# Performance work log

Hardware: AMD Instinct MI355X
Metric: run time of the kernel (lower is better)

Reference implementation:

```python
import jax, jax.numpy as jnp
import numpy as np

N = 100000       # nodes
E = 1600000      # edges
NFEAT = 256
NHID = 128
NCLASS = 40


def setup_inputs() -> dict:
    key = jax.random.key(0)
    ks = jax.random.split(key, 7)
    x = jax.random.normal(ks[0], (N, NFEAT), dtype=jnp.float32)
    edge_index = jax.random.randint(ks[1], (2, E), 0, N, dtype=jnp.int32)
    edge_weight = jax.random.uniform(ks[2], (E,), dtype=jnp.float32)
    # Glorot-style init as in PyG GCNConv.reset_parameters
    W1 = jax.random.normal(ks[3], (NFEAT, NHID), dtype=jnp.float32) * np.float32(1.0 / np.sqrt(NFEAT))
    b1 = jnp.zeros((NHID,), dtype=jnp.float32)
    W2 = jax.random.normal(ks[4], (NHID, NCLASS), dtype=jnp.float32) * np.float32(1.0 / np.sqrt(NHID))
    b2 = jnp.zeros((NCLASS,), dtype=jnp.float32)
    return {"x": x, "edge_index": edge_index, "edge_weight": edge_weight,
            "W1": W1, "b1": b1, "W2": W2, "b2": b2}


def gcn_conv(x, W, b, src, dst, ew, n):
    """PyG GCNConv with add_self_loops=True (self-loop weight 1), sym norm.

    Self-loop contribution is added analytically (norm_ii = deg_i^-1) so we
    never materialize the augmented edge list.
    """
    xw = x @ W                                            # [n, out]
    deg = jax.ops.segment_sum(ew, dst, num_segments=n) + 1.0  # +1 self loop
    dinv = jnp.where(deg > 0, jax.lax.rsqrt(deg), 0.0)    # deg^-1/2
    norm = dinv[src] * ew * dinv[dst]                     # [E]
    agg = jax.ops.segment_sum(norm[:, None] * xw[src], dst, num_segments=n)
    agg = agg + (dinv * dinv)[:, None] * xw               # self-loop term
    return agg + b


def reference(x, edge_index, edge_weight, W1, b1, W2, b2):
    n = x.shape[0]
    src, dst = edge_index[0], edge_index[1]
    h = jax.nn.relu(gcn_conv(x, W1, b1, src, dst, edge_weight, n))
    # dropout is identity in eval mode
    h = gcn_conv(h, W2, b2, src, dst, edge_weight, n)
    nrm = jnp.linalg.norm(h, axis=-1, keepdims=True)      # F.normalize p=2
    return h / jnp.maximum(nrm, 1e-12)
```

## Files before the change

kernel.cpp:

```cpp
#include <hip/hip_runtime.h>


typedef unsigned short u16;
typedef unsigned long long u64;
typedef __attribute__((ext_vector_type(8))) short short8;
typedef __attribute__((ext_vector_type(4))) float f32x4;

#define FIXSCALE 4194304.0f
#define HW2S 64
#define NSLAB 384
#define MAXBUCK 832

static __device__ inline u16 f2bf(float f) {
    unsigned u = __float_as_uint(f);
    return (u16)((u + 0x7fffu + ((u >> 16) & 1u)) >> 16);
}
static __device__ inline float bf2f(u16 h) { return __uint_as_float(((unsigned)h) << 16); }

__launch_bounds__(256)
__global__ void k_count(const int* __restrict__ dst, int* __restrict__ cnt1,
                        int E, int EPB, int NBUCK) {
    __shared__ int cnt[MAXBUCK];
    int b = blockIdx.x;
    for (int j = threadIdx.x; j < NBUCK; j += 256) cnt[j] = 0;
    __syncthreads();
    int beg = b * EPB, end = min(beg + EPB, E);
    for (int i = beg + threadIdx.x; i < end; i += 256)
        atomicAdd(&cnt[dst[i] >> 7], 1);
    __syncthreads();
    for (int j = threadIdx.x; j < NBUCK; j += 256)
        cnt1[(size_t)b * NBUCK + j] = cnt[j];
}

__launch_bounds__(NSLAB)
__global__ void k_s2a(int* __restrict__ cnt1, int* __restrict__ colTot, int NBUCK) {
    __shared__ int s[NSLAB];
    int j = blockIdx.x;
    int t = threadIdx.x;
    int v = cnt1[(size_t)t * NBUCK + j];
    s[t] = v;
    __syncthreads();
    for (int off = 1; off < NSLAB; off <<= 1) {
        int u = (t >= off) ? s[t - off] : 0;
        __syncthreads();
        s[t] += u;
        __syncthreads();
    }
    cnt1[(size_t)t * NBUCK + j] = s[t] - v;
    if (t == NSLAB - 1) colTot[j] = s[t];
}

__launch_bounds__(1024)
__global__ void k_s2b(const int* __restrict__ colTot, int* __restrict__ bucketBase,
                      int* __restrict__ rowp, int NBUCK, int N, int E) {
    __shared__ int s[1024];
    int t = threadIdx.x;
    int v = (t < NBUCK) ? colTot[t] : 0;
    s[t] = v;
    __syncthreads();
    for (int off = 1; off < 1024; off <<= 1) {
        int u = (t >= off) ? s[t - off] : 0;
        __syncthreads();
        s[t] += u;
        __syncthreads();
    }
    if (t < NBUCK) bucketBase[t] = s[t] - v;
    if (t == NBUCK - 1) bucketBase[NBUCK] = s[t];
    if (t == 0) rowp[N] = E;
}

__launch_bounds__(256)
__global__ void k_fat(const float* __restrict__ x, const u16* __restrict__ wt_hi,
                      u16* __restrict__ xw1, int N,
                      const int* __restrict__ src, const int* __restrict__ dst,
                      const float* __restrict__ ew, const int* __restrict__ cnt1,
                      const int* __restrict__ bucketBase, u64* __restrict__ tmp,
                      int E, int gB, int EPB, int NBUCK) {
    __shared__ __align__(16) u16 S[10240];
    u16* Ah = S;
    u16* Bh = S + 5120;

    if (blockIdx.x >= gB) {
        int* ldsOff = (int*)S;
        int b = blockIdx.x - gB, t = threadIdx.x;
        for (int j = t; j < NBUCK; j += 256)
            ldsOff[j] = bucketBase[j] + cnt1[(size_t)b * NBUCK + j];
        __syncthreads();
        int beg = b * EPB, end = min(beg + EPB, E);
        for (int i = beg + t; i < end; i += 256) {
            int d = dst[i];
            int slot = atomicAdd(&ldsOff[d >> 7], 1);
            unsigned fix = (unsigned)__float2uint_rn(ew[i] * FIXSCALE);
            tmp[slot] = ((u64)(unsigned)src[i] << 30) | ((u64)(d & 127) << 23) | fix;
        }
        return;
    }

    const int t = threadIdx.x;
    const int w = t >> 6;
    const int lane = t & 63;
    const int lrow = lane & 15;
    const int q = lane >> 4;
    const int lk = q * 8;
    const int row0 = blockIdx.x * 128;

    int rA[4], cA[4];
    const float* pA[4];
    bool okA[4];
#pragma unroll
    for (int i = 0; i < 4; ++i) {
        int flat = t + i * 256;
        rA[i] = flat >> 3;
        cA[i] = flat & 7;
        int gr = row0 + rA[i];
        okA[i] = gr < N;
        pA[i] = x + (size_t)min(gr, N - 1) * 256 + cA[i] * 4;
    }
    int nB[2], cB[2];
    const u16* pB[2];
#pragma unroll
    for (int i = 0; i < 2; ++i) {
        int flat = t + i * 256;
        nB[i] = flat >> 2;
        cB[i] = flat & 3;
        pB[i] = wt_hi + (size_t)nB[i] * 256 + cB[i] * 8;
    }

    float4 ra[4];
    short8 rb[2];
#pragma unroll
    for (int i = 0; i < 4; ++i)
        ra[i] = okA[i] ? *(const float4*)(pA[i]) : make_float4(0.f, 0.f, 0.f, 0.f);
#pragma unroll
    for (int i = 0; i < 2; ++i) rb[i] = *(const short8*)(pB[i]);

    f32x4 acc[2][8] = {};

    for (int kt = 0; kt < 8; ++kt) {
#pragma unroll
        for (int i = 0; i < 4; ++i) {
            ushort4 vh;
            vh.x = f2bf(ra[i].x);
            vh.y = f2bf(ra[i].y);
            vh.z = f2bf(ra[i].z);
            vh.w = f2bf(ra[i].w);
            *(ushort4*)(Ah + rA[i] * 40 + cA[i] * 4) = vh;
        }
#pragma unroll
        for (int i = 0; i < 2; ++i)
            *(short8*)(Bh + nB[i] * 40 + cB[i] * 8) = rb[i];
        __syncthreads();

        if (kt < 7) {
#pragma unroll
            for (int i = 0; i < 4; ++i)
                ra[i] = okA[i] ? *(const float4*)(pA[i] + (kt + 1) * 32)
                               : make_float4(0.f, 0.f, 0.f, 0.f);
#pragma unroll
            for (int i = 0; i < 2; ++i)
                rb[i] = *(const short8*)(pB[i] + (kt + 1) * 32);
        }

        short8 a0 = *(const short8*)(Ah + (w * 32 + lrow) * 40 + lk);
        short8 a1 = *(const short8*)(Ah + (w * 32 + 16 + lrow) * 40 + lk);
#pragma unroll
        for (int ni = 0; ni < 8; ++ni) {
            short8 bh = *(const short8*)(Bh + (ni * 16 + lrow) * 40 + lk);
            acc[0][ni] = __builtin_amdgcn_mfma_f32_16x16x32_bf16(a0, bh, acc[0][ni], 0, 0, 0);
            acc[1][ni] = __builtin_amdgcn_mfma_f32_16x16x32_bf16(a1, bh, acc[1][ni], 0, 0, 0);
        }
        __syncthreads();
    }

#pragma unroll
    for (int mi = 0; mi < 2; ++mi) {
        if (mi) __syncthreads();
#pragma unroll
        for (int r = 0; r < 4; ++r)
#pragma unroll
            for (int ni = 0; ni < 8; ++ni)
                S[(w * 16 + q * 4 + r) * 136 + lrow + ni * 16] = f2bf(acc[mi][ni][r]);
        __syncthreads();
        int l = t >> 2;
        int grow = row0 + (l >> 4) * 32 + mi * 16 + (l & 15);
        if (grow < N) {
#pragma unroll
            for (int c = 0; c < 4; ++c) {
                int col = (t & 3) * 8 + c * 32;
                *(short8*)(xw1 + (size_t)grow * 128 + col) =
                    *(const short8*)(S + l * 136 + col);
            }
        }
    }
}

__launch_bounds__(256)
__global__ void k_s4(const u64* __restrict__ tmp, const int* __restrict__ bucketBase,
                     int* __restrict__ rowp, float* __restrict__ dinv,
                     int2* __restrict__ entries, int N) {
    __shared__ int cnt[128];
    __shared__ unsigned degfix[128];
    __shared__ int sc[128];
    __shared__ int nextOff[128];
    __shared__ float dl[128];
    int k = blockIdx.x, t = threadIdx.x;
    int base = bucketBase[k], endb = bucketBase[k + 1];
    if (t < 128) { cnt[t] = 0; degfix[t] = 0; }
    __syncthreads();
    for (int i = base + t; i < endb; i += 256) {
        u64 r = tmp[i];
        int lid = (int)(r >> 23) & 127;
        atomicAdd(&cnt[lid], 1);
        atomicAdd(&degfix[lid], (unsigned)(r & 0x7fffff));
    }
    __syncthreads();
    if (t < 128) sc[t] = cnt[t];
    __syncthreads();
    for (int off = 1; off < 128; off <<= 1) {
        int u = 0;
        if (t < 128 && t >= off) u = sc[t - off];
        __syncthreads();
        if (t < 128) sc[t] += u;
        __syncthreads();
    }
    if (t < 128) {
        int off0 = base + sc[t] - cnt[t];
        nextOff[t] = off0;
        float di = rsqrtf((float)degfix[t] * (1.0f / FIXSCALE) + 1.0f);
        dl[t] = di;
        int gn = k * 128 + t;
        if (gn < N) { rowp[gn] = off0; dinv[gn] = di; }
    }
    __syncthreads();
    for (int i = base + t; i < endb; i += 256) {
        u64 r = tmp[i];
        int lid = (int)(r >> 23) & 127;
        int slot = atomicAdd(&nextOff[lid], 1);
        float ew = (float)(unsigned)(r & 0x7fffff) * (1.0f / FIXSCALE);
        float w = ew * dl[lid];
        entries[slot] = make_int2((int)(r >> 30), __float_as_int(w));
    }
}

__global__ void k_wsplit(const float* __restrict__ W1, u16* __restrict__ wt_hi) {
    int idx = blockIdx.x * 256 + threadIdx.x;
    if (idx < 256 * 128) {
        int n = idx & 127, k = idx >> 7;
        wt_hi[n * 256 + k] = f2bf(W1[idx]);
    }
}

__launch_bounds__(256)
__global__ void k_gather1(const u16* __restrict__ xw1, const int2* __restrict__ entries,
                          const int* __restrict__ row, const float* __restrict__ dinv,
                          u16* __restrict__ agg1, int N) {
    int g = (blockIdx.x * 256 + threadIdx.x) >> 5;
    if (g >= N) return;
    int j = (threadIdx.x & 31) * 4;
    float di = dinv[g];
    float d2 = di * di;
    ushort4 sv = *(const ushort4*)(xw1 + (size_t)g * 128 + j);
    float4 acc = make_float4(d2 * bf2f(sv.x), d2 * bf2f(sv.y),
                             d2 * bf2f(sv.z), d2 * bf2f(sv.w));
    int e = row[g], end = row[g + 1];
    for (; e + 4 <= end; e += 4) {
        int2 e0 = entries[e];
        int2 e1 = entries[e + 1];
        int2 e2 = entries[e + 2];
        int2 e3 = entries[e + 3];
        ushort4 v0 = *(const ushort4*)(xw1 + (size_t)e0.x * 128 + j);
        ushort4 v1 = *(const ushort4*)(xw1 + (size_t)e1.x * 128 + j);
        ushort4 v2 = *(const ushort4*)(xw1 + (size_t)e2.x * 128 + j);
        ushort4 v3 = *(const ushort4*)(xw1 + (size_t)e3.x * 128 + j);
        float w0 = __int_as_float(e0.y) * dinv[e0.x];
        float w1 = __int_as_float(e1.y) * dinv[e1.x];
        float w2 = __int_as_float(e2.y) * dinv[e2.x];
        float w3 = __int_as_float(e3.y) * dinv[e3.x];
        acc.x += w0 * bf2f(v0.x) + w1 * bf2f(v1.x) + w2 * bf2f(v2.x) + w3 * bf2f(v3.x);
        acc.y += w0 * bf2f(v0.y) + w1 * bf2f(v1.y) + w2 * bf2f(v2.y) + w3 * bf2f(v3.y);
        acc.z += w0 * bf2f(v0.z) + w1 * bf2f(v1.z) + w2 * bf2f(v2.z) + w3 * bf2f(v3.z);
        acc.w += w0 * bf2f(v0.w) + w1 * bf2f(v1.w) + w2 * bf2f(v2.w) + w3 * bf2f(v3.w);
    }
    for (; e < end; ++e) {
        int2 e0 = entries[e];
        ushort4 v0 = *(const ushort4*)(xw1 + (size_t)e0.x * 128 + j);
        float w0 = __int_as_float(e0.y) * dinv[e0.x];
        acc.x += w0 * bf2f(v0.x);
        acc.y += w0 * bf2f(v0.y);
        acc.z += w0 * bf2f(v0.z);
        acc.w += w0 * bf2f(v0.w);
    }
    ushort4 o;
    o.x = f2bf(acc.x);
    o.y = f2bf(acc.y);
    o.z = f2bf(acc.z);
    o.w = f2bf(acc.w);
    *(ushort4*)(agg1 + (size_t)g * 128 + j) = o;
}

__launch_bounds__(320)
__global__ void k_gemm2(const u16* __restrict__ agg1, const float* __restrict__ W2,
                        const float* __restrict__ b1, const float* __restrict__ dinv,
                        u16* __restrict__ hw2, int N) {
    __shared__ float As[64 * 132];
    __shared__ float Bs[128 * 40];
    const int t = threadIdx.x;
    const int row0 = blockIdx.x * 64;

    for (int flat = t; flat < 128 * 40; flat += 320) Bs[flat] = W2[flat];

#pragma unroll
    for (int i = 0; i < 7; ++i) {
        int flat = t + i * 320;
        if (flat < 2048) {
            int r = flat >> 5, c4 = flat & 31;
            int gr = row0 + r;
            float4 v = make_float4(0.f, 0.f, 0.f, 0.f);
            if (gr < N) {
                ushort4 s = *(const ushort4*)(agg1 + (size_t)gr * 128 + c4 * 4);
                float4 bb = *(const float4*)(b1 + c4 * 4);
                v.x = fmaxf(bf2f(s.x) + bb.x, 0.f);
                v.y = fmaxf(bf2f(s.y) + bb.y, 0.f);
                v.z = fmaxf(bf2f(s.z) + bb.z, 0.f);
                v.w = fmaxf(bf2f(s.w) + bb.w, 0.f);
            }
            *(float4*)(As + r * 132 + c4 * 4) = v;
        }
    }
    __syncthreads();

    const int tx = t % 40;
    const int ty = t / 40;
    float acc[8];
#pragma unroll
    for (int r = 0; r < 8; ++r) acc[r] = 0.f;
    for (int k = 0; k < 128; ++k) {
        float b = Bs[k * 40 + tx];
#pragma unroll
        for (int r = 0; r < 8; ++r) acc[r] += As[(ty * 8 + r) * 132 + k] * b;
    }
#pragma unroll
    for (int r = 0; r < 8; ++r) {
        int gr = row0 + ty * 8 + r;
        if (gr < N) hw2[(size_t)gr * HW2S + tx] = f2bf(dinv[gr] * acc[r]);
    }
    for (int idx = t; idx < 64 * 24; idx += 320) {
        int r = idx / 24, c = 40 + idx % 24;
        int gr = row0 + r;
        if (gr < N) hw2[(size_t)gr * HW2S + c] = 0;
    }
}

__launch_bounds__(256)
__global__ void k_gather2(const u16* __restrict__ hw2, const int2* __restrict__ entries,
                          const int* __restrict__ row, const float* __restrict__ dinv,
                          const float* __restrict__ b2, float* __restrict__ out, int N) {
    int g = (blockIdx.x * 256 + threadIdx.x) >> 3;
    if (g >= N) return;
    int l = threadIdx.x & 7;
    int c0 = l * 8;
    float di = dinv[g];
    float bb[8];
#pragma unroll
    for (int k = 0; k < 8; ++k) bb[k] = (c0 + k < 40) ? b2[c0 + k] : 0.f;

    float acc[8];
    {
        short8 sv = *(const short8*)(hw2 + (size_t)g * HW2S + c0);
#pragma unroll
        for (int k = 0; k < 8; ++k) acc[k] = di * bf2f((u16)sv[k]) + bb[k];
    }
    int e = row[g], end = row[g + 1];
    for (; e + 2 <= end; e += 2) {
        int2 e0 = entries[e];
        int2 e1 = entries[e + 1];
        float w0 = __int_as_float(e0.y);
        float w1 = __int_as_float(e1.y);
        short8 v0 = *(const short8*)(hw2 + (size_t)e0.x * HW2S + c0);
        short8 v1 = *(const short8*)(hw2 + (size_t)e1.x * HW2S + c0);
#pragma unroll
        for (int k = 0; k < 8; ++k)
            acc[k] += w0 * bf2f((u16)v0[k]) + w1 * bf2f((u16)v1[k]);
    }
    if (e < end) {
        int2 e0 = entries[e];
        float w0 = __int_as_float(e0.y);
        short8 v0 = *(const short8*)(hw2 + (size_t)e0.x * HW2S + c0);
#pragma unroll
        for (int k = 0; k < 8; ++k) acc[k] += w0 * bf2f((u16)v0[k]);
    }
    float ss = 0.f;
#pragma unroll
    for (int k = 0; k < 8; ++k) ss += acc[k] * acc[k];
    ss += __shfl_xor(ss, 1);
    ss += __shfl_xor(ss, 2);
    ss += __shfl_xor(ss, 4);
    float inv = 1.f / fmaxf(sqrtf(ss), 1e-12f);
    if (l < 5) {
        float* q = out + (size_t)g * 40 + c0;
        *(float4*)(q)     = make_float4(acc[0] * inv, acc[1] * inv, acc[2] * inv, acc[3] * inv);
        *(float4*)(q + 4) = make_float4(acc[4] * inv, acc[5] * inv, acc[6] * inv, acc[7] * inv);
    }
}

extern "C" void kernel_launch(void* const* d_in, const int* in_sizes, int n_in,
                              void* d_out, int out_size, void* d_ws, size_t ws_size,
                              hipStream_t stream) {
    const float* x   = (const float*)d_in[0];
    const int*   ei  = (const int*)d_in[1];
    const float* ew  = (const float*)d_in[2];
    const float* W1  = (const float*)d_in[3];
    const float* b1  = (const float*)d_in[4];
    const float* W2  = (const float*)d_in[5];
    const float* b2  = (const float*)d_in[6];
    float* out = (float*)d_out;

    const int N = in_sizes[0] / 256;
    const int E = in_sizes[2];
    const int* src = ei;
    const int* dst = ei + E;
    const int NBUCK = (N + 127) >> 7;
    const int EPB = (E + NSLAB - 1) / NSLAB;

    char* ws = (char*)d_ws;
    size_t off = 0;
    auto take = [&](size_t bytes) -> void* {
        void* p = (void*)(ws + off);
        off += (bytes + 255) & ~(size_t)255;
        return p;
    };
    int*   cnt1    = (int*)take((size_t)NSLAB * NBUCK * 4);
    int*   colTot  = (int*)take((size_t)NBUCK * 4);
    int*   bucketBase = (int*)take((size_t)(NBUCK + 1) * 4);
    int*   rowp    = (int*)take((size_t)(N + 1) * 4);
    float* dinv    = (float*)take((size_t)N * 4);
    u64*   tmp     = (u64*)take((size_t)E * 8);
    int2*  entries = (int2*)take((size_t)E * 8);
    u16*   wt_hi   = (u16*)take((size_t)128 * 256 * 2);
    u16*   xw1     = (u16*)take((size_t)N * 128 * 2);
    u16*   agg1    = (u16*)take((size_t)N * 128 * 2);
    u16*   hw2     = (u16*)take((size_t)N * HW2S * 2);

    k_wsplit<<<(256 * 128 + 255) / 256, 256, 0, stream>>>(W1, wt_hi);
    k_count<<<NSLAB, 256, 0, stream>>>(dst, cnt1, E, EPB, NBUCK);
    k_s2a<<<NBUCK, NSLAB, 0, stream>>>(cnt1, colTot, NBUCK);
    k_s2b<<<1, 1024, 0, stream>>>(colTot, bucketBase, rowp, NBUCK, N, E);

    const int gB = (N + 127) / 128;
    k_fat<<<gB + NSLAB, 256, 0, stream>>>(x, wt_hi, xw1, N,
                                          src, dst, ew, cnt1, bucketBase, tmp,
                                          E, gB, EPB, NBUCK);

    k_s4<<<NBUCK, 256, 0, stream>>>(tmp, bucketBase, rowp, dinv, entries, N);

    k_gather1<<<(N * 32 + 255) / 256, 256, 0, stream>>>(xw1, entries, rowp, dinv, agg1, N);
    k_gemm2<<<(N + 63) / 64, 320, 0, stream>>>(agg1, W2, b1, dinv, hw2, N);
    k_gather2<<<(N * 8 + 255) / 256, 256, 0, stream>>>(hw2, entries, rowp, dinv, b2, out, N);
}
```

Measured before the change: 228.3 us.

## Raise slab count and batch column scan over 16 buckets per block

Increases the number of edge slabs, giving more blocks in the count and scatter phases. It also rewrites the per-bucket column scan so each block loads a 16-bucket tile of the slab-by-bucket count matrix into shared memory with coalesced reads. Sixteen threads then do serial exclusive scans down the slabs, replacing one block per bucket running a barrier-heavy log-step scan. This trades a long serial loop of 640 shared-memory steps per column for fewer blocks, fewer barriers and coalesced global accesses.

```diff
diff --git a/kernel.cpp b/kernel.cpp
--- a/kernel.cpp
+++ b/kernel.cpp
@@ -8,8 +8,9 @@
 
 #define FIXSCALE 4194304.0f
 #define HW2S 64
-#define NSLAB 384
+#define NSLAB 640
 #define MAXBUCK 832
+#define SB 16
 
 static __device__ inline u16 f2bf(float f) {
     unsigned u = __float_as_uint(f);
@@ -32,22 +33,31 @@
         cnt1[(size_t)b * NBUCK + j] = cnt[j];
 }
 
-__launch_bounds__(NSLAB)
+__launch_bounds__(256)
 __global__ void k_s2a(int* __restrict__ cnt1, int* __restrict__ colTot, int NBUCK) {
-    __shared__ int s[NSLAB];
-    int j = blockIdx.x;
+    __shared__ int d[NSLAB][SB + 1];
+    int j0 = blockIdx.x * SB;
+    int nj = min(SB, NBUCK - j0);
     int t = threadIdx.x;
-    int v = cnt1[(size_t)t * NBUCK + j];
-    s[t] = v;
-    __syncthreads();
-    for (int off = 1; off < NSLAB; off <<= 1) {
-        int u = (t >= off) ? s[t - off] : 0;
-        __syncthreads();
-        s[t] += u;
-        __syncthreads();
-    }
-    cnt1[(size_t)t * NBUCK + j] = s[t] - v;
-    if (t == NSLAB - 1) colTot[j] = s[t];
+    for (int f = t; f < NSLAB * SB; f += 256) {
+        int b = f >> 4, jj = f & 15;
+        d[b][jj] = (jj < nj) ? cnt1[(size_t)b * NBUCK + j0 + jj] : 0;
+    }
+    __syncthreads();
+    if (t < SB) {
+        int run = 0;
+        for (int b = 0; b < NSLAB; ++b) {
+            int v = d[b][t];
+            d[b][t] = run;
+            run += v;
+        }
+        if (t < nj) colTot[j0 + t] = run;
+    }
+    __syncthreads();
+    for (int f = t; f < NSLAB * SB; f += 256) {
+        int b = f >> 4, jj = f & 15;
+        if (jj < nj) cnt1[(size_t)b * NBUCK + j0 + jj] = d[b][jj];
+    }
 }
 
 __launch_bounds__(1024)
@@ -443,7 +453,7 @@
 
     k_wsplit<<<(256 * 128 + 255) / 256, 256, 0, stream>>>(W1, wt_hi);
     k_count<<<NSLAB, 256, 0, stream>>>(dst, cnt1, E, EPB, NBUCK);
-    k_s2a<<<NBUCK, NSLAB, 0, stream>>>(cnt1, colTot, NBUCK);
+    k_s2a<<<(NBUCK + SB - 1) / SB, 256, 0, stream>>>(cnt1, colTot, NBUCK);
     k_s2b<<<1, 1024, 0, stream>>>(colTot, bucketBase, rowp, NBUCK, N, E);
 
     const int gB = (N + 127) / 128;
```

Result: slower. 243.4 us (+6.6%).
